# Optimization experiments

Measured on AMD Instinct MI355X. Metric: run time of the kernel, lower is better.

## Reference

```python
import jax, jax.numpy as jnp
import numpy as np

B, N = 32, 512
N_DIM, N_P, N_K = 128, 3, 2
F0_DIM = N_DIM * N_P            # 384
CAT_DIM = N_DIM * (N_K + 1) * N_P  # 1152


def setup_inputs() -> dict:
    key = jax.random.key(0)
    ks = jax.random.split(key, 12)
    s = 0.05
    return {
        "loc": jax.random.uniform(ks[0], (B, N, 2), dtype=jnp.float32),
        "deadline": jax.random.uniform(ks[1], (B, N), dtype=jnp.float32),
        "workload": jax.random.uniform(ks[2], (B, N), dtype=jnp.float32),
        "depot": jax.random.uniform(ks[3], (B, 1, 2), dtype=jnp.float32),
        "W_init": jax.random.normal(ks[4], (3, F0_DIM), dtype=jnp.float32) * s,
        "b_init": jnp.zeros((F0_DIM,), jnp.float32),
        "W_dep": jax.random.normal(ks[5], (2, N_DIM), dtype=jnp.float32) * s,
        "b_dep": jnp.zeros((N_DIM,), jnp.float32),
        "W_g1": jax.random.normal(ks[6], (CAT_DIM, N_DIM), dtype=jnp.float32) * s,
        "b_g1": jnp.zeros((N_DIM,), jnp.float32),
        "W_g2": jax.random.normal(ks[7], (CAT_DIM, N_DIM), dtype=jnp.float32) * s,
        "b_g2": jnp.zeros((N_DIM,), jnp.float32),
        "W_g3": jax.random.normal(ks[8], (CAT_DIM, N_DIM), dtype=jnp.float32) * s,
        "b_g3": jnp.zeros((N_DIM,), jnp.float32),
        "gamma": jnp.ones((F0_DIM,), jnp.float32),
        "beta": jnp.zeros((F0_DIM,), jnp.float32),
        "W_F": jax.random.normal(ks[9], (F0_DIM, N_DIM), dtype=jnp.float32) * s,
        "b_F": jnp.zeros((N_DIM,), jnp.float32),
    }


def _forward(loc, deadline, workload, depot, W_init, b_init, W_dep, b_dep,
             W_g1, b_g1, W_g2, b_g2, W_g3, b_g3, gamma, beta, W_F, b_F):
    # X = [loc, deadline/deadline.max()] -> [B,N,3] (workload is concatenated then dropped in original)
    X = jnp.concatenate([loc, (deadline / deadline.max())[..., None]], axis=-1)
    n = X.shape[1]
    # pairwise squared distances [B,N,N]
    d2 = ((X[:, :, None, :] - X[:, None, :, :]) ** 2).sum(-1)
    off = ~jnp.eye(n, dtype=bool)                      # off-diagonal mask
    d2_safe = jnp.where(off, d2, 1.0)
    A = jnp.where(off, 1.0 / jnp.sqrt(d2_safe), 0.0)   # A = 1/dist off-diag, 0 on diag
    A = jnp.where(jnp.isnan(A), 0.0, A)                # A[A!=A]=0
    A = A / A.max()                                    # global max-normalize
    deg = A.sum(-1) - 1.0                              # (A.sum(-1) - 1)
    L = jnp.eye(n, dtype=A.dtype) * deg[:, None, :] - A  # D - A (diag = deg)
    L2 = L @ L

    F0 = X @ W_init + b_init                           # [B,N,384]
    F0_sq = F0 * F0
    F0_cu = F0 * F0_sq

    def prop(F):
        return jnp.concatenate([F, L @ F, L2 @ F], axis=-1)  # [B,N,1152]

    g1 = prop(F0) @ W_g1 + b_g1
    g2 = prop(F0_sq) @ W_g2 + b_g2
    g3 = prop(F0_cu) @ W_g3 + b_g3
    F1 = jnp.concatenate([g1, g2, g3], axis=-1)        # [B,N,384]
    F1 = jax.nn.leaky_relu(F1) + F0

    # BatchNorm1d (training mode): stats over flattened (B*N) samples, biased var
    flat = F1.reshape(-1, F1.shape[-1])
    mu = flat.mean(0)
    var = ((flat - mu) ** 2).mean(0)
    F1 = (F1 - mu) / jnp.sqrt(var + 1e-5) * gamma + beta

    F_final = jax.nn.leaky_relu(F1 @ W_F + b_F)        # [B,N,128]
    dep = depot @ W_dep + b_dep                        # [B,1,128]
    h = jnp.concatenate([dep, F_final], axis=1)        # [B,N+1,128]
    return h, h.mean(axis=1)


def reference(loc, deadline, workload, depot, W_init, b_init, W_dep, b_dep,
              W_g1, b_g1, W_g2, b_g2, W_g3, b_g3, gamma, beta, W_F, b_F):
    return _forward(loc, deadline, workload, depot, W_init, b_init, W_dep, b_dep,
                    W_g1, b_g1, W_g2, b_g2, W_g3, b_g3, gamma, beta, W_F, b_F)
```

## Files before the change

### kernel.cpp

```cpp
#include <hip/hip_runtime.h>

#define LEAKY(x) ((x) > 0.0f ? (x) : 0.01f * (x))

typedef __attribute__((ext_vector_type(8))) short bf16x8;
typedef __attribute__((ext_vector_type(4))) float f32x4;
typedef __attribute__((ext_vector_type(4))) unsigned short u16x4;

__device__ __forceinline__ unsigned short f2bf(float f) {
    unsigned int u = __float_as_uint(f);
    unsigned int r = (u + 0x7fffu + ((u >> 16) & 1u)) >> 16;
    return (unsigned short)r;
}
__device__ __forceinline__ float bf2f(unsigned short u) {
    return __uint_as_float(((unsigned int)u) << 16);
}

__device__ __forceinline__ void dma16(const unsigned short* g, unsigned short* l) {
    __builtin_amdgcn_global_load_lds(
        (const __attribute__((address_space(1))) void*)g,
        (__attribute__((address_space(3))) void*)l, 16, 0, 0);
}


__global__ void k_dmax(const float* __restrict__ deadline, float* __restrict__ dmax) {
    __shared__ float red[256];
    int t = threadIdx.x;
    float m = -1e30f;
    for (int i = t; i < 16384; i += 256) m = fmaxf(m, deadline[i]);
    red[t] = m; __syncthreads();
    for (int s = 128; s > 0; s >>= 1) {
        if (t < s) red[t] = fmaxf(red[t], red[t + s]);
        __syncthreads();
    }
    if (t == 0) *dmax = red[0];
}

__global__ __launch_bounds__(256) void k_buildR(const float* __restrict__ loc,
                                                const float* __restrict__ deadline,
                                                const float* __restrict__ dmaxv,
                                                float* __restrict__ R,
                                                float* __restrict__ rowsum, float* __restrict__ pmax) {
    int blk = blockIdx.x;
    int wave = threadIdx.x >> 6, lane = threadIdx.x & 63;
    int bi = blk * 4 + wave;
    int b = bi >> 9, i = bi & 511;
    float invd = 1.0f / (*dmaxv);
    const float* lb = loc + b * 1024;
    const float* db = deadline + b * 512;
    float xi = lb[i * 2], yi = lb[i * 2 + 1], zi = db[i] * invd;
    float lsum = 0.f, lmax = 0.f;
    float* Rrow = R + (size_t)bi * 512;
    for (int j = lane; j < 512; j += 64) {
        float d0 = xi - lb[j * 2], d1 = yi - lb[j * 2 + 1], d2 = zi - db[j] * invd;
        float dd = d0 * d0 + d1 * d1 + d2 * d2;
        float r = (j == i) ? 0.f : rsqrtf(dd);
        Rrow[j] = r;
        lsum += r; lmax = fmaxf(lmax, r);
    }
    for (int off = 32; off > 0; off >>= 1) {
        lsum += __shfl_down(lsum, off);
        lmax = fmaxf(lmax, __shfl_down(lmax, off));
    }
    __shared__ float smax[4];
    if (lane == 0) { rowsum[bi] = lsum; smax[wave] = lmax; }
    __syncthreads();
    if (threadIdx.x == 0) pmax[blk] = fmaxf(fmaxf(smax[0], smax[1]), fmaxf(smax[2], smax[3]));
}

__global__ void k_amax(const float* __restrict__ pmax, float* __restrict__ amaxf) {
    __shared__ float red[256];
    int t = threadIdx.x;
    float m = 0.f;
    for (int i = t; i < 4096; i += 256) m = fmaxf(m, pmax[i]);
    red[t] = m; __syncthreads();
    for (int s = 128; s > 0; s >>= 1) {
        if (t < s) red[t] = fmaxf(red[t], red[t + s]);
        __syncthreads();
    }
    if (t == 0) *amaxf = red[0];
}

__global__ void k_buildL(const float* __restrict__ R, const float* __restrict__ rowsum,
                         const float* __restrict__ amaxf, unsigned short* __restrict__ Lb) {
    int id = blockIdx.x * 256 + threadIdx.x;
    float inv = 1.0f / (*amaxf);
    size_t e = (size_t)id * 4;
    size_t bi = e >> 9;
    int i = (int)(bi & 511);
    int j0 = (int)(e & 511);
    float4 rv = *(const float4*)(R + e);
    float diag = rowsum[bi] * inv - 1.0f;
    u16x4 o;
    o[0] = f2bf(i == j0     ? diag : -rv.x * inv);
    o[1] = f2bf(i == j0 + 1 ? diag : -rv.y * inv);
    o[2] = f2bf(i == j0 + 2 ? diag : -rv.z * inv);
    o[3] = f2bf(i == j0 + 3 ? diag : -rv.w * inv);
    *(u16x4*)(Lb + e) = o;
}

__global__ void k_F0pow(const float* __restrict__ loc, const float* __restrict__ deadline,
                        const float* __restrict__ dmaxv,
                        const float* __restrict__ Wi, const float* __restrict__ bi_,
                        unsigned short* __restrict__ P1, unsigned short* __restrict__ P2,
                        unsigned short* __restrict__ P3) {
    int id = blockIdx.x * 256 + threadIdx.x;
    int row = id / 96, c4 = (id % 96) * 4;
    float x0 = loc[row * 2], x1 = loc[row * 2 + 1], x2 = deadline[row] / (*dmaxv);
    float4 w0 = *(const float4*)(Wi + c4);
    float4 w1 = *(const float4*)(Wi + 384 + c4);
    float4 w2 = *(const float4*)(Wi + 768 + c4);
    float4 bb = *(const float4*)(bi_ + c4);
    float f[4] = {x0 * w0.x + x1 * w1.x + x2 * w2.x + bb.x,
                  x0 * w0.y + x1 * w1.y + x2 * w2.y + bb.y,
                  x0 * w0.z + x1 * w1.z + x2 * w2.z + bb.z,
                  x0 * w0.w + x1 * w1.w + x2 * w2.w + bb.w};
    u16x4 o1, o2, o3;
#pragma unroll
    for (int j = 0; j < 4; j++) {
        o1[j] = f2bf(f[j]); o2[j] = f2bf(f[j] * f[j]); o3[j] = f2bf(f[j] * f[j] * f[j]);
    }
    size_t e = (size_t)row * 384 + c4;
    *(u16x4*)(P1 + e) = o1; *(u16x4*)(P2 + e) = o2; *(u16x4*)(P3 + e) = o3;
}

__global__ void k_prepW(const float* __restrict__ Wg1, const float* __restrict__ Wg2,
                        const float* __restrict__ Wg3, unsigned short* __restrict__ WgT) {
    int id = blockIdx.x * 256 + threadIdx.x;
    int combo = id / 49152, rem = id % 49152;
    int n = rem / 384, k = rem % 384;
    int kp = combo / 3, part = combo % 3;
    const float* W = (kp == 0) ? Wg1 : (kp == 1 ? Wg2 : Wg3);
    WgT[id] = f2bf(W[(part * 384 + k) * 128 + n]);
}


__device__ __forceinline__ void phase128x64(
    const unsigned short* __restrict__ Ab, int Astr,
    const unsigned short* __restrict__ Bb, int Bstr,
    int kiters, unsigned short* AsL, unsigned short* BsL,
    f32x4 (&acc)[4][2], int t)
{
    const int wave = t >> 6, lane = t & 63;
    const int wm = wave >> 1, wn = wave & 1;
    const int quad = lane >> 4, l16 = lane & 15;
    const int lrow = lane >> 2, lkq = (lane & 3) * 8;
    for (int s = 0; s < kiters; s++) {
        __syncthreads();
        int k0 = s * 64;
#pragma unroll
        for (int h = 0; h < 2; h++) {
            const unsigned short* Ah = Ab + k0 + h * 32 + lkq;
            unsigned short* Ap = AsL + h * 4096;
            dma16(Ah + (size_t)(wave * 16 + lrow) * Astr, Ap + wave * 512);
            dma16(Ah + (size_t)((wave + 4) * 16 + lrow) * Astr, Ap + (wave + 4) * 512);
            dma16(Bb + k0 + h * 32 + lkq + (size_t)(wave * 16 + lrow) * Bstr,
                  BsL + h * 2048 + wave * 512);
        }
        __syncthreads();
#pragma unroll
        for (int h = 0; h < 2; h++) {
            bf16x8 af[4], bfr[2];
#pragma unroll
            for (int i = 0; i < 4; i++)
                af[i] = *(const bf16x8*)(AsL + h * 4096 + (wm * 64 + i * 16 + l16) * 32 + quad * 8);
#pragma unroll
            for (int n = 0; n < 2; n++)
                bfr[n] = *(const bf16x8*)(BsL + h * 2048 + (wn * 32 + n * 16 + l16) * 32 + quad * 8);
#pragma unroll
            for (int i = 0; i < 4; i++)
#pragma unroll
                for (int n = 0; n < 2; n++)
                    acc[i][n] = __builtin_amdgcn_mfma_f32_16x16x32_bf16(af[i], bfr[n], acc[i][n], 0, 0, 0);
        }
    }
}

__device__ __forceinline__ void phase64x64(
    const unsigned short* __restrict__ Ab, int Astr,
    const unsigned short* __restrict__ Bb, int Bstr,
    int kiters, unsigned short* AsL, unsigned short* BsL,
    f32x4 (&acc)[2][2], int t)
{
    const int wave = t >> 6, lane = t & 63;
    const int wm = wave >> 1, wn = wave & 1;
    const int quad = lane >> 4, l16 = lane & 15;
    const int lrow = lane >> 2, lkq = (lane & 3) * 8;
    for (int s = 0; s < kiters; s++) {
        __syncthreads();
        int k0 = s * 64;
#pragma unroll
        for (int h = 0; h < 2; h++) {
            dma16(Ab + k0 + h * 32 + lkq + (size_t)(wave * 16 + lrow) * Astr,
                  AsL + h * 2048 + wave * 512);
            dma16(Bb + k0 + h * 32 + lkq + (size_t)(wave * 16 + lrow) * Bstr,
                  BsL + h * 2048 + wave * 512);
        }
        __syncthreads();
#pragma unroll
        for (int h = 0; h < 2; h++) {
            bf16x8 af[2], bfr[2];
#pragma unroll
            for (int i = 0; i < 2; i++)
                af[i] = *(const bf16x8*)(AsL + h * 2048 + (wm * 32 + i * 16 + l16) * 32 + quad * 8);
#pragma unroll
            for (int n = 0; n < 2; n++)
                bfr[n] = *(const bf16x8*)(BsL + h * 2048 + (wn * 32 + n * 16 + l16) * 32 + quad * 8);
#pragma unroll
            for (int i = 0; i < 2; i++)
#pragma unroll
                for (int n = 0; n < 2; n++)
                    acc[i][n] = __builtin_amdgcn_mfma_f32_16x16x32_bf16(af[i], bfr[n], acc[i][n], 0, 0, 0);
        }
    }
}

__global__ __launch_bounds__(256) void k_ygemmT(
    const unsigned short* __restrict__ WgT,
    const unsigned short* __restrict__ P1, const unsigned short* __restrict__ P2,
    const unsigned short* __restrict__ P3, unsigned short* __restrict__ Y2T)
{
    __shared__ unsigned short AsL[8192], BsL[4096];
    const int t = threadIdx.x;
    const int kp = blockIdx.x;
    const int nb = blockIdx.y;
    const int b = blockIdx.z;
    const unsigned short* P = (kp == 0) ? P1 : (kp == 1 ? P2 : P3);
    f32x4 acc[4][2];
#pragma unroll
    for (int i = 0; i < 4; i++)
#pragma unroll
        for (int n = 0; n < 2; n++) acc[i][n] = (f32x4){0.f, 0.f, 0.f, 0.f};
    phase128x64(WgT + (size_t)(kp * 3 + 2) * 49152, 384,
                P + ((size_t)b * 512 + nb * 64) * 384, 384, 6, AsL, BsL, acc, t);

    const int wave = t >> 6, lane = t & 63;
    const int wm = wave >> 1, wn = wave & 1;
    const int quad = lane >> 4, l16 = lane & 15;
#pragma unroll
    for (int i = 0; i < 4; i++)
#pragma unroll
        for (int n = 0; n < 2; n++) {
            int g = kp * 128 + wm * 64 + i * 16 + quad * 4;
            int node = nb * 64 + wn * 32 + n * 16 + l16;
#pragma unroll
            for (int r = 0; r < 4; r++)
                Y2T[((size_t)b * 384 + g + r) * 512 + node] = f2bf(acc[i][n][r]);
        }
}

__global__ __launch_bounds__(256) void k_lg1T(
    const unsigned short* __restrict__ Lb, const unsigned short* __restrict__ Y2T,
    const unsigned short* __restrict__ WgT,
    const unsigned short* __restrict__ P1, const unsigned short* __restrict__ P2,
    const unsigned short* __restrict__ P3, unsigned short* __restrict__ ZT)
{
    __shared__ unsigned short AsL[8192], BsL[4096];
    const int t = threadIdx.x;
    const int kp = blockIdx.x;
    const int nb = blockIdx.y;
    const int b = blockIdx.z;
    const unsigned short* P = (kp == 0) ? P1 : (kp == 1 ? P2 : P3);
    f32x4 acc[4][2];
#pragma unroll
    for (int i = 0; i < 4; i++)
#pragma unroll
        for (int n = 0; n < 2; n++) acc[i][n] = (f32x4){0.f, 0.f, 0.f, 0.f};
    phase128x64(Y2T + (size_t)b * 196608 + (size_t)kp * 128 * 512, 512,
                Lb + (size_t)b * 262144 + (size_t)nb * 64 * 512, 512, 8, AsL, BsL, acc, t);
    phase128x64(WgT + (size_t)(kp * 3 + 1) * 49152, 384,
                P + ((size_t)b * 512 + nb * 64) * 384, 384, 6, AsL, BsL, acc, t);

    const int wave = t >> 6, lane = t & 63;
    const int wm = wave >> 1, wn = wave & 1;
    const int quad = lane >> 4, l16 = lane & 15;
#pragma unroll
    for (int i = 0; i < 4; i++)
#pragma unroll
        for (int n = 0; n < 2; n++) {
            int g = kp * 128 + wm * 64 + i * 16 + quad * 4;
            int node = nb * 64 + wn * 32 + n * 16 + l16;
#pragma unroll
            for (int r = 0; r < 4; r++)
                ZT[((size_t)b * 384 + g + r) * 512 + node] = f2bf(acc[i][n][r]);
        }
}

__global__ __launch_bounds__(256) void k_lg2(
    const unsigned short* __restrict__ Lb, const unsigned short* __restrict__ ZT,
    const unsigned short* __restrict__ WgT,
    const unsigned short* __restrict__ P1, const unsigned short* __restrict__ P2,
    const unsigned short* __restrict__ P3,
    const float* __restrict__ bg1, const float* __restrict__ bg2, const float* __restrict__ bg3,
    unsigned short* __restrict__ F1b, float* __restrict__ bn1, float* __restrict__ bn2)
{
    __shared__ unsigned short AsL[8192], BsL[4096];
    __shared__ float bnS[64], bnQ[64];
    const int t = threadIdx.x;
    const int mb = blockIdx.x;
    const int gt = blockIdx.y;
    const int b = blockIdx.z;
    const int kp = gt >> 1;
    if (t < 64) { bnS[t] = 0.f; bnQ[t] = 0.f; }
    const unsigned short* P = (kp == 0) ? P1 : (kp == 1 ? P2 : P3);
    f32x4 acc[4][2];
#pragma unroll
    for (int i = 0; i < 4; i++)
#pragma unroll
        for (int n = 0; n < 2; n++) acc[i][n] = (f32x4){0.f, 0.f, 0.f, 0.f};
    phase128x64(Lb + (size_t)b * 262144 + (size_t)mb * 128 * 512, 512,
                ZT + (size_t)b * 196608 + (size_t)gt * 64 * 512, 512, 8, AsL, BsL, acc, t);
    phase128x64(P + ((size_t)b * 512 + mb * 128) * 384, 384,
                WgT + (size_t)(kp * 3) * 49152 + (size_t)(gt & 1) * 64 * 384, 384, 6, AsL, BsL, acc, t);

    const int wave = t >> 6, lane = t & 63;
    const int wm = wave >> 1, wn = wave & 1;
    const int quad = lane >> 4, l16 = lane & 15;
    const float* bg = (kp == 0) ? bg1 : (kp == 1 ? bg2 : bg3);
    float ls1[2], ls2[2];
#pragma unroll
    for (int n = 0; n < 2; n++) { ls1[n] = 0.f; ls2[n] = 0.f; }
#pragma unroll
    for (int i = 0; i < 4; i++) {
        int rowl = mb * 128 + wm * 64 + i * 16 + quad * 4;
        size_t rowg = (size_t)b * 512 + rowl;
#pragma unroll
        for (int n = 0; n < 2; n++) {
            int nloc = wn * 32 + n * 16 + l16;
            int g = gt * 64 + nloc;
            float bias = bg[(gt & 1) * 64 + nloc];
#pragma unroll
            for (int r = 0; r < 4; r++) {
                size_t idx = (rowg + r) * 384 + g;
                float c = acc[i][n][r] + bias;
                float v = LEAKY(c) + bf2f(P1[idx]);
                F1b[idx] = f2bf(v);
                ls1[n] += v; ls2[n] += v * v;
            }
        }
    }
#pragma unroll
    for (int n = 0; n < 2; n++) {
        int nloc = wn * 32 + n * 16 + l16;
        atomicAdd(&bnS[nloc], ls1[n]);
        atomicAdd(&bnQ[nloc], ls2[n]);
    }
    __syncthreads();
    if (t < 64) {
        atomicAdd(&bn1[gt * 64 + t], bnS[t]);
        atomicAdd(&bn2[gt * 64 + t], bnQ[t]);
    }
}

__global__ __launch_bounds__(384) void k_bnfin_beff(
    const float* __restrict__ bn1, const float* __restrict__ bn2,
    const float* __restrict__ gamma, const float* __restrict__ beta,
    const float* __restrict__ WF, const float* __restrict__ bF,
    float* __restrict__ sS, float* __restrict__ beffv)
{
    __shared__ float ttL[384];
    int c = threadIdx.x;
    float mu = bn1[c] * (1.f / 16384.f);
    float var = bn2[c] * (1.f / 16384.f) - mu * mu;
    float sc = gamma[c] / sqrtf(var + 1e-5f);
    sS[c] = sc;
    ttL[c] = beta[c] - mu * sc;
    __syncthreads();
    if (c < 128) {
        float a = bF[c];
        for (int k = 0; k < 384; k++) a += ttL[k] * WF[k * 128 + c];
        beffv[c] = a;
    }
}

__global__ void k_fold(const float* __restrict__ WF, const float* __restrict__ sS,
                       unsigned short* __restrict__ WFsT) {
    int id = blockIdx.x * 256 + threadIdx.x;
    int n = id / 384, k = id % 384;
    WFsT[id] = f2bf(WF[k * 128 + n] * sS[k]);
}

__global__ __launch_bounds__(256) void k_fgemm(
    const unsigned short* __restrict__ F1b, const unsigned short* __restrict__ WFsT,
    const float* __restrict__ beffv, float* __restrict__ out, float* __restrict__ msum)
{
    __shared__ unsigned short AsL[4096], BsL[4096];
    __shared__ float msS[64];
    const int t = threadIdx.x;
    const int mb = blockIdx.x;
    const int nt = blockIdx.y;
    if (t < 64) msS[t] = 0.f;
    f32x4 acc[2][2];
#pragma unroll
    for (int i = 0; i < 2; i++)
#pragma unroll
        for (int n = 0; n < 2; n++) acc[i][n] = (f32x4){0.f, 0.f, 0.f, 0.f};
    phase64x64(F1b + (size_t)mb * 64 * 384, 384,
               WFsT + (size_t)nt * 64 * 384, 384, 6, AsL, BsL, acc, t);

    const int wave = t >> 6, lane = t & 63;
    const int wm = wave >> 1, wn = wave & 1;
    const int quad = lane >> 4, l16 = lane & 15;
    const int bloc = mb >> 3;
    float ls[2];
#pragma unroll
    for (int n = 0; n < 2; n++) ls[n] = 0.f;
#pragma unroll
    for (int i = 0; i < 2; i++) {
        int rowg = mb * 64 + wm * 32 + i * 16 + quad * 4;
        int nd = rowg & 511;
#pragma unroll
        for (int n = 0; n < 2; n++) {
            int nloc = wn * 32 + n * 16 + l16;
            int col = nt * 64 + nloc;
            float bb = beffv[col];
#pragma unroll
            for (int r = 0; r < 4; r++) {
                float x = acc[i][n][r] + bb;
                float v = LEAKY(x);
                out[(size_t)bloc * 65664 + (size_t)(nd + r + 1) * 128 + col] = v;
                ls[n] += v;
            }
        }
    }
#pragma unroll
    for (int n = 0; n < 2; n++) atomicAdd(&msS[wn * 32 + n * 16 + l16], ls[n]);
    __syncthreads();
    if (t < 64) atomicAdd(&msum[bloc * 128 + nt * 64 + t], msS[t]);
}

__global__ void k_meandep(const float* __restrict__ depot, const float* __restrict__ Wd,
                          const float* __restrict__ bd, const float* __restrict__ msum,
                          float* __restrict__ out) {
    int id = blockIdx.x * 256 + threadIdx.x;
    int b = id >> 7, o = id & 127;
    float dep = depot[b * 2] * Wd[o] + depot[b * 2 + 1] * Wd[128 + o] + bd[o];
    out[(size_t)b * 65664 + o] = dep;
    out[2101248 + id] = (msum[id] + dep) * (1.0f / 513.0f);
}


extern "C" void kernel_launch(void* const* d_in, const int* in_sizes, int n_in,
                              void* d_out, int out_size, void* d_ws, size_t ws_size,
                              hipStream_t stream) {
    const float* loc      = (const float*)d_in[0];
    const float* deadline = (const float*)d_in[1];
    const float* depot    = (const float*)d_in[3];
    const float* W_init   = (const float*)d_in[4];
    const float* b_init   = (const float*)d_in[5];
    const float* W_dep    = (const float*)d_in[6];
    const float* b_dep    = (const float*)d_in[7];
    const float* W_g1     = (const float*)d_in[8];
    const float* b_g1     = (const float*)d_in[9];
    const float* W_g2     = (const float*)d_in[10];
    const float* b_g2     = (const float*)d_in[11];
    const float* W_g3     = (const float*)d_in[12];
    const float* b_g3     = (const float*)d_in[13];
    const float* gamma    = (const float*)d_in[14];
    const float* beta     = (const float*)d_in[15];
    const float* W_F      = (const float*)d_in[16];
    const float* b_F      = (const float*)d_in[17];
    float* out = (float*)d_out;
    float* ws  = (float*)d_ws;

    float* dmaxv  = ws + 0;
    float* amaxf  = ws + 4;
    float* bn1    = ws + 8;
    float* bn2    = ws + 392;
    float* msum   = ws + 776;
    float* rowsum = ws + 4872;
    float* pmax   = ws + 21256;
    float* sS     = ws + 25352;
    float* beffv  = ws + 25736;
    float* R      = ws + 25864;
    unsigned short* Lb   = (unsigned short*)(ws + 8414472);
    unsigned short* P1   = (unsigned short*)(ws + 12608776);
    unsigned short* P2   = (unsigned short*)(ws + 15754504);
    unsigned short* P3   = (unsigned short*)(ws + 18900232);
    unsigned short* WgT  = (unsigned short*)(ws + 22045960);
    unsigned short* WFsT = (unsigned short*)(ws + 22267144);
    unsigned short* Y2T  = (unsigned short*)(ws + 22291720);
    unsigned short* ZT   = (unsigned short*)(ws + 25437448);
    unsigned short* F1b  = (unsigned short*)(ws + 28583176);

    hipMemsetAsync(bn1, 0, (384 + 384 + 4096) * sizeof(float), stream);

    k_dmax<<<1, 256, 0, stream>>>(deadline, dmaxv);
    k_buildR<<<4096, 256, 0, stream>>>(loc, deadline, dmaxv, R, rowsum, pmax);
    k_amax<<<1, 256, 0, stream>>>(pmax, amaxf);
    k_buildL<<<8192, 256, 0, stream>>>(R, rowsum, amaxf, Lb);
    k_F0pow<<<6144, 256, 0, stream>>>(loc, deadline, dmaxv, W_init, b_init, P1, P2, P3);
    k_prepW<<<1728, 256, 0, stream>>>(W_g1, W_g2, W_g3, WgT);

    k_ygemmT<<<dim3(3, 8, 32), 256, 0, stream>>>(WgT, P1, P2, P3, Y2T);
    k_lg1T<<<dim3(3, 8, 32), 256, 0, stream>>>(Lb, Y2T, WgT, P1, P2, P3, ZT);
    k_lg2<<<dim3(4, 6, 32), 256, 0, stream>>>(Lb, ZT, WgT, P1, P2, P3,
                                              b_g1, b_g2, b_g3, F1b, bn1, bn2);

    k_bnfin_beff<<<1, 384, 0, stream>>>(bn1, bn2, gamma, beta, W_F, b_F, sS, beffv);
    k_fold<<<192, 256, 0, stream>>>(W_F, sS, WFsT);
    k_fgemm<<<dim3(256, 2), 256, 0, stream>>>(F1b, WFsT, beffv, out, msum);
    k_meandep<<<16, 256, 0, stream>>>(depot, W_dep, b_dep, msum, out);
}
```

Measured before the change: 265.7 us.

## Double-buffer GEMM tiles via registers, swizzle LDS, recompute distances, remap grids

The GEMM inner loops swap direct global-to-LDS DMA for register prefetch into double-buffered, XOR-swizzled shared memory, so the next K-tile loads while MFMAs run and there is one barrier per step. The two GEMM phases in each kernel are merged into one continuous pipeline. The dense fp32 distance matrix R is no longer written; the L builder recomputes rsqrt distances from loc and deadline, which removes a large global write and read. Grids are flattened with batch as the fastest index to change block scheduling and cache locality, at the cost of doubled shared memory per block.

```diff
diff --git a/kernel.cpp b/kernel.cpp
--- a/kernel.cpp
+++ b/kernel.cpp
@@ -4,6 +4,7 @@
 
 typedef __attribute__((ext_vector_type(8))) short bf16x8;
 typedef __attribute__((ext_vector_type(4))) float f32x4;
+typedef __attribute__((ext_vector_type(8))) unsigned short u16x8;
 typedef __attribute__((ext_vector_type(4))) unsigned short u16x4;
 
 __device__ __forceinline__ unsigned short f2bf(float f) {
@@ -13,12 +14,6 @@
 }
 __device__ __forceinline__ float bf2f(unsigned short u) {
     return __uint_as_float(((unsigned int)u) << 16);
-}
-
-__device__ __forceinline__ void dma16(const unsigned short* g, unsigned short* l) {
-    __builtin_amdgcn_global_load_lds(
-        (const __attribute__((address_space(1))) void*)g,
-        (__attribute__((address_space(3))) void*)l, 16, 0, 0);
 }
 
 
@@ -35,11 +30,10 @@
     if (t == 0) *dmax = red[0];
 }
 
-__global__ __launch_bounds__(256) void k_buildR(const float* __restrict__ loc,
-                                                const float* __restrict__ deadline,
-                                                const float* __restrict__ dmaxv,
-                                                float* __restrict__ R,
-                                                float* __restrict__ rowsum, float* __restrict__ pmax) {
+__global__ __launch_bounds__(256) void k_rowstats(const float* __restrict__ loc,
+                                                  const float* __restrict__ deadline,
+                                                  const float* __restrict__ dmaxv,
+                                                  float* __restrict__ rowsum, float* __restrict__ pmax) {
     int blk = blockIdx.x;
     int wave = threadIdx.x >> 6, lane = threadIdx.x & 63;
     int bi = blk * 4 + wave;
@@ -49,12 +43,10 @@
     const float* db = deadline + b * 512;
     float xi = lb[i * 2], yi = lb[i * 2 + 1], zi = db[i] * invd;
     float lsum = 0.f, lmax = 0.f;
-    float* Rrow = R + (size_t)bi * 512;
     for (int j = lane; j < 512; j += 64) {
         float d0 = xi - lb[j * 2], d1 = yi - lb[j * 2 + 1], d2 = zi - db[j] * invd;
         float dd = d0 * d0 + d1 * d1 + d2 * d2;
         float r = (j == i) ? 0.f : rsqrtf(dd);
-        Rrow[j] = r;
         lsum += r; lmax = fmaxf(lmax, r);
     }
     for (int off = 32; off > 0; off >>= 1) {
@@ -80,21 +72,35 @@
     if (t == 0) *amaxf = red[0];
 }
 
-__global__ void k_buildL(const float* __restrict__ R, const float* __restrict__ rowsum,
+__global__ void k_buildL(const float* __restrict__ loc, const float* __restrict__ deadline,
+                         const float* __restrict__ dmaxv, const float* __restrict__ rowsum,
                          const float* __restrict__ amaxf, unsigned short* __restrict__ Lb) {
     int id = blockIdx.x * 256 + threadIdx.x;
     float inv = 1.0f / (*amaxf);
+    float invd = 1.0f / (*dmaxv);
     size_t e = (size_t)id * 4;
     size_t bi = e >> 9;
+    int b = (int)(bi >> 9);
     int i = (int)(bi & 511);
     int j0 = (int)(e & 511);
-    float4 rv = *(const float4*)(R + e);
+    const float* lb = loc + b * 1024;
+    const float* db = deadline + b * 512;
+    float xi = lb[i * 2], yi = lb[i * 2 + 1], zi = db[i] * invd;
+    float4 l01 = *(const float4*)(lb + j0 * 2);
+    float4 l23 = *(const float4*)(lb + j0 * 2 + 4);
+    float4 dj = *(const float4*)(db + j0);
     float diag = rowsum[bi] * inv - 1.0f;
+    float jx[4] = {l01.x, l01.z, l23.x, l23.z};
+    float jy[4] = {l01.y, l01.w, l23.y, l23.w};
+    float jz[4] = {dj.x * invd, dj.y * invd, dj.z * invd, dj.w * invd};
     u16x4 o;
-    o[0] = f2bf(i == j0     ? diag : -rv.x * inv);
-    o[1] = f2bf(i == j0 + 1 ? diag : -rv.y * inv);
-    o[2] = f2bf(i == j0 + 2 ? diag : -rv.z * inv);
-    o[3] = f2bf(i == j0 + 3 ? diag : -rv.w * inv);
+#pragma unroll
+    for (int j = 0; j < 4; j++) {
+        float d0 = xi - jx[j], d1 = yi - jy[j], d2 = zi - jz[j];
+        float dd = d0 * d0 + d1 * d1 + d2 * d2;
+        float v = (i == j0 + j) ? diag : -rsqrtf(dd) * inv;
+        o[j] = f2bf(v);
+    }
     *(u16x4*)(Lb + e) = o;
 }
 
@@ -134,83 +140,114 @@
 }
 
 
-__device__ __forceinline__ void phase128x64(
-    const unsigned short* __restrict__ Ab, int Astr,
-    const unsigned short* __restrict__ Bb, int Bstr,
-    int kiters, unsigned short* AsL, unsigned short* BsL,
+__device__ __forceinline__ void pipe128x64(
+    const unsigned short* __restrict__ A0, int As0, const unsigned short* __restrict__ B0, int Bs0, int it0,
+    const unsigned short* __restrict__ A1, int As1, const unsigned short* __restrict__ B1, int Bs1, int it1,
+    unsigned short* AsL, unsigned short* BsL,
     f32x4 (&acc)[4][2], int t)
 {
-    const int wave = t >> 6, lane = t & 63;
+    const int lane = t & 63, wave = t >> 6;
     const int wm = wave >> 1, wn = wave & 1;
     const int quad = lane >> 4, l16 = lane & 15;
-    const int lrow = lane >> 2, lkq = (lane & 3) * 8;
-    for (int s = 0; s < kiters; s++) {
+    const int ra = t >> 1, ca = (t & 1) * 4;
+    const int rb = t >> 2, cb = (t & 3) * 2;
+    const unsigned short* Ar0 = A0 + (size_t)ra * As0;
+    const unsigned short* Ar1 = A1 ? (A1 + (size_t)ra * As1) : Ar0;
+    const unsigned short* Br0 = B0 + (size_t)rb * Bs0;
+    const unsigned short* Br1 = B1 ? (B1 + (size_t)rb * Bs1) : Br0;
+    const int total = it0 + it1;
+    u16x8 pa[4], pb[2];
+#pragma unroll
+    for (int j = 0; j < 4; j++) pa[j] = *(const u16x8*)(Ar0 + (ca + j) * 8);
+#pragma unroll
+    for (int j = 0; j < 2; j++) pb[j] = *(const u16x8*)(Br0 + (cb + j) * 8);
+    int buf = 0;
+    for (int s = 0; s < total; s++) {
+#pragma unroll
+        for (int j = 0; j < 4; j++)
+            *(u16x8*)(AsL + buf * 8192 + ra * 64 + (((ca + j) ^ (ra & 7)) * 8)) = pa[j];
+#pragma unroll
+        for (int j = 0; j < 2; j++)
+            *(u16x8*)(BsL + buf * 4096 + rb * 64 + (((cb + j) ^ (rb & 7)) * 8)) = pb[j];
         __syncthreads();
-        int k0 = s * 64;
-#pragma unroll
-        for (int h = 0; h < 2; h++) {
-            const unsigned short* Ah = Ab + k0 + h * 32 + lkq;
-            unsigned short* Ap = AsL + h * 4096;
-            dma16(Ah + (size_t)(wave * 16 + lrow) * Astr, Ap + wave * 512);
-            dma16(Ah + (size_t)((wave + 4) * 16 + lrow) * Astr, Ap + (wave + 4) * 512);
-            dma16(Bb + k0 + h * 32 + lkq + (size_t)(wave * 16 + lrow) * Bstr,
-                  BsL + h * 2048 + wave * 512);
-        }
-        __syncthreads();
+        if (s + 1 < total) {
+            int s2 = s + 1;
+            int sg = (s2 >= it0);
+            int k0 = (sg ? (s2 - it0) : s2) * 64;
+            const unsigned short* Ar = sg ? Ar1 : Ar0;
+            const unsigned short* Br = sg ? Br1 : Br0;
+#pragma unroll
+            for (int j = 0; j < 4; j++) pa[j] = *(const u16x8*)(Ar + k0 + (ca + j) * 8);
+#pragma unroll
+            for (int j = 0; j < 2; j++) pb[j] = *(const u16x8*)(Br + k0 + (cb + j) * 8);
+        }
 #pragma unroll
         for (int h = 0; h < 2; h++) {
             bf16x8 af[4], bfr[2];
+            int phys = ((h * 4 + quad) ^ (l16 & 7)) * 8;
 #pragma unroll
             for (int i = 0; i < 4; i++)
-                af[i] = *(const bf16x8*)(AsL + h * 4096 + (wm * 64 + i * 16 + l16) * 32 + quad * 8);
+                af[i] = *(const bf16x8*)(AsL + buf * 8192 + (wm * 64 + i * 16 + l16) * 64 + phys);
 #pragma unroll
             for (int n = 0; n < 2; n++)
-                bfr[n] = *(const bf16x8*)(BsL + h * 2048 + (wn * 32 + n * 16 + l16) * 32 + quad * 8);
+                bfr[n] = *(const bf16x8*)(BsL + buf * 4096 + (wn * 32 + n * 16 + l16) * 64 + phys);
 #pragma unroll
             for (int i = 0; i < 4; i++)
 #pragma unroll
                 for (int n = 0; n < 2; n++)
                     acc[i][n] = __builtin_amdgcn_mfma_f32_16x16x32_bf16(af[i], bfr[n], acc[i][n], 0, 0, 0);
         }
-    }
-}
-
-__device__ __forceinline__ void phase64x64(
-    const unsigned short* __restrict__ Ab, int Astr,
-    const unsigned short* __restrict__ Bb, int Bstr,
-    int kiters, unsigned short* AsL, unsigned short* BsL,
+        buf ^= 1;
+    }
+}
+
+__device__ __forceinline__ void pipe64x64(
+    const unsigned short* __restrict__ A0, int As0, const unsigned short* __restrict__ B0, int Bs0, int it0,
+    unsigned short* AsL, unsigned short* BsL,
     f32x4 (&acc)[2][2], int t)
 {
-    const int wave = t >> 6, lane = t & 63;
+    const int lane = t & 63, wave = t >> 6;
     const int wm = wave >> 1, wn = wave & 1;
     const int quad = lane >> 4, l16 = lane & 15;
-    const int lrow = lane >> 2, lkq = (lane & 3) * 8;
-    for (int s = 0; s < kiters; s++) {
+    const int rb = t >> 2, cb = (t & 3) * 2;
+    const unsigned short* Ar0 = A0 + (size_t)rb * As0;
+    const unsigned short* Br0 = B0 + (size_t)rb * Bs0;
+    u16x8 pa[2], pb[2];
+#pragma unroll
+    for (int j = 0; j < 2; j++) { pa[j] = *(const u16x8*)(Ar0 + (cb + j) * 8);
+                                  pb[j] = *(const u16x8*)(Br0 + (cb + j) * 8); }
+    int buf = 0;
+    for (int s = 0; s < it0; s++) {
+#pragma unroll
+        for (int j = 0; j < 2; j++) {
+            int phys = ((cb + j) ^ (rb & 7)) * 8;
+            *(u16x8*)(AsL + buf * 4096 + rb * 64 + phys) = pa[j];
+            *(u16x8*)(BsL + buf * 4096 + rb * 64 + phys) = pb[j];
+        }
         __syncthreads();
-        int k0 = s * 64;
-#pragma unroll
-        for (int h = 0; h < 2; h++) {
-            dma16(Ab + k0 + h * 32 + lkq + (size_t)(wave * 16 + lrow) * Astr,
-                  AsL + h * 2048 + wave * 512);
-            dma16(Bb + k0 + h * 32 + lkq + (size_t)(wave * 16 + lrow) * Bstr,
-                  BsL + h * 2048 + wave * 512);
-        }
-        __syncthreads();
+        if (s + 1 < it0) {
+            int k0 = (s + 1) * 64;
+#pragma unroll
+            for (int j = 0; j < 2; j++) { pa[j] = *(const u16x8*)(Ar0 + k0 + (cb + j) * 8);
+                                          pb[j] = *(const u16x8*)(Br0 + k0 + (cb + j) * 8); }
+        }
 #pragma unroll
         for (int h = 0; h < 2; h++) {
             bf16x8 af[2], bfr[2];
+            int phys = ((h * 4 + quad) ^ (l16 & 7)) * 8;
 #pragma unroll
             for (int i = 0; i < 2; i++)
-                af[i] = *(const bf16x8*)(AsL + h * 2048 + (wm * 32 + i * 16 + l16) * 32 + quad * 8);
+                af[i] = *(const bf16x8*)(AsL + buf * 4096 + (wm * 32 + i * 16 + l16) * 64 + phys);
 #pragma unroll
             for (int n = 0; n < 2; n++)
-                bfr[n] = *(const bf16x8*)(BsL + h * 2048 + (wn * 32 + n * 16 + l16) * 32 + quad * 8);
+                bfr[n] = *(const bf16x8*)(BsL + buf * 4096 + (wn * 32 + n * 16 + l16) * 64 + phys);
 #pragma unroll
             for (int i = 0; i < 2; i++)
 #pragma unroll
                 for (int n = 0; n < 2; n++)
                     acc[i][n] = __builtin_amdgcn_mfma_f32_16x16x32_bf16(af[i], bfr[n], acc[i][n], 0, 0, 0);
         }
+        buf ^= 1;
     }
 }
 
@@ -219,19 +256,20 @@
     const unsigned short* __restrict__ P1, const unsigned short* __restrict__ P2,
     const unsigned short* __restrict__ P3, unsigned short* __restrict__ Y2T)
 {
-    __shared__ unsigned short AsL[8192], BsL[4096];
+    __shared__ unsigned short AsL[16384], BsL[8192];
     const int t = threadIdx.x;
-    const int kp = blockIdx.x;
-    const int nb = blockIdx.y;
-    const int b = blockIdx.z;
+    const int id = blockIdx.x;
+    const int b = id & 31, tt = id >> 5;
+    const int kp = tt >> 3, nb = tt & 7;
     const unsigned short* P = (kp == 0) ? P1 : (kp == 1 ? P2 : P3);
     f32x4 acc[4][2];
 #pragma unroll
     for (int i = 0; i < 4; i++)
 #pragma unroll
         for (int n = 0; n < 2; n++) acc[i][n] = (f32x4){0.f, 0.f, 0.f, 0.f};
-    phase128x64(WgT + (size_t)(kp * 3 + 2) * 49152, 384,
-                P + ((size_t)b * 512 + nb * 64) * 384, 384, 6, AsL, BsL, acc, t);
+    pipe128x64(WgT + (size_t)(kp * 3 + 2) * 49152, 384,
+               P + ((size_t)b * 512 + nb * 64) * 384, 384, 6,
+               nullptr, 0, nullptr, 0, 0, AsL, BsL, acc, t);
 
     const int wave = t >> 6, lane = t & 63;
     const int wm = wave >> 1, wn = wave & 1;
@@ -254,21 +292,21 @@
     const unsigned short* __restrict__ P1, const unsigned short* __restrict__ P2,
     const unsigned short* __restrict__ P3, unsigned short* __restrict__ ZT)
 {
-    __shared__ unsigned short AsL[8192], BsL[4096];
+    __shared__ unsigned short AsL[16384], BsL[8192];
     const int t = threadIdx.x;
-    const int kp = blockIdx.x;
-    const int nb = blockIdx.y;
-    const int b = blockIdx.z;
+    const int id = blockIdx.x;
+    const int b = id & 31, tt = id >> 5;
+    const int kp = tt >> 3, nb = tt & 7;
     const unsigned short* P = (kp == 0) ? P1 : (kp == 1 ? P2 : P3);
     f32x4 acc[4][2];
 #pragma unroll
     for (int i = 0; i < 4; i++)
 #pragma unroll
         for (int n = 0; n < 2; n++) acc[i][n] = (f32x4){0.f, 0.f, 0.f, 0.f};
-    phase128x64(Y2T + (size_t)b * 196608 + (size_t)kp * 128 * 512, 512,
-                Lb + (size_t)b * 262144 + (size_t)nb * 64 * 512, 512, 8, AsL, BsL, acc, t);
-    phase128x64(WgT + (size_t)(kp * 3 + 1) * 49152, 384,
-                P + ((size_t)b * 512 + nb * 64) * 384, 384, 6, AsL, BsL, acc, t);
+    pipe128x64(Y2T + (size_t)b * 196608 + (size_t)kp * 128 * 512, 512,
+               Lb + (size_t)b * 262144 + (size_t)nb * 64 * 512, 512, 8,
+               WgT + (size_t)(kp * 3 + 1) * 49152, 384,
+               P + ((size_t)b * 512 + nb * 64) * 384, 384, 6, AsL, BsL, acc, t);
 
     const int wave = t >> 6, lane = t & 63;
     const int wm = wave >> 1, wn = wave & 1;
@@ -293,12 +331,12 @@
     const float* __restrict__ bg1, const float* __restrict__ bg2, const float* __restrict__ bg3,
     unsigned short* __restrict__ F1b, float* __restrict__ bn1, float* __restrict__ bn2)
 {
-    __shared__ unsigned short AsL[8192], BsL[4096];
+    __shared__ unsigned short AsL[16384], BsL[8192];
     __shared__ float bnS[64], bnQ[64];
     const int t = threadIdx.x;
-    const int mb = blockIdx.x;
-    const int gt = blockIdx.y;
-    const int b = blockIdx.z;
+    const int id = blockIdx.x;
+    const int b = id & 31, tt = id >> 5;
+    const int mb = tt & 3, gt = tt >> 2;
     const int kp = gt >> 1;
     if (t < 64) { bnS[t] = 0.f; bnQ[t] = 0.f; }
     const unsigned short* P = (kp == 0) ? P1 : (kp == 1 ? P2 : P3);
@@ -307,10 +345,11 @@
     for (int i = 0; i < 4; i++)
 #pragma unroll
         for (int n = 0; n < 2; n++) acc[i][n] = (f32x4){0.f, 0.f, 0.f, 0.f};
-    phase128x64(Lb + (size_t)b * 262144 + (size_t)mb * 128 * 512, 512,
-                ZT + (size_t)b * 196608 + (size_t)gt * 64 * 512, 512, 8, AsL, BsL, acc, t);
-    phase128x64(P + ((size_t)b * 512 + mb * 128) * 384, 384,
-                WgT + (size_t)(kp * 3) * 49152 + (size_t)(gt & 1) * 64 * 384, 384, 6, AsL, BsL, acc, t);
+    pipe128x64(Lb + (size_t)b * 262144 + (size_t)mb * 128 * 512, 512,
+               ZT + (size_t)b * 196608 + (size_t)gt * 64 * 512, 512, 8,
+               P + ((size_t)b * 512 + mb * 128) * 384, 384,
+               WgT + (size_t)(kp * 3) * 49152 + (size_t)(gt & 1) * 64 * 384, 384, 6,
+               AsL, BsL, acc, t);
 
     const int wave = t >> 6, lane = t & 63;
     const int wm = wave >> 1, wn = wave & 1;
@@ -383,41 +422,39 @@
     const unsigned short* __restrict__ F1b, const unsigned short* __restrict__ WFsT,
     const float* __restrict__ beffv, float* __restrict__ out, float* __restrict__ msum)
 {
-    __shared__ unsigned short AsL[4096], BsL[4096];
+    __shared__ unsigned short AsL[8192], BsL[8192];
     __shared__ float msS[64];
     const int t = threadIdx.x;
-    const int mb = blockIdx.x;
-    const int nt = blockIdx.y;
+    const int id = blockIdx.x;
+    const int b = id & 31, tt = id >> 5;
+    const int seg = tt >> 1, nt = tt & 1;
     if (t < 64) msS[t] = 0.f;
     f32x4 acc[2][2];
 #pragma unroll
     for (int i = 0; i < 2; i++)
 #pragma unroll
         for (int n = 0; n < 2; n++) acc[i][n] = (f32x4){0.f, 0.f, 0.f, 0.f};
-    phase64x64(F1b + (size_t)mb * 64 * 384, 384,
-               WFsT + (size_t)nt * 64 * 384, 384, 6, AsL, BsL, acc, t);
+    pipe64x64(F1b + ((size_t)b * 512 + seg * 64) * 384, 384,
+              WFsT + (size_t)nt * 64 * 384, 384, 6, AsL, BsL, acc, t);
 
     const int wave = t >> 6, lane = t & 63;
     const int wm = wave >> 1, wn = wave & 1;
     const int quad = lane >> 4, l16 = lane & 15;
-    const int bloc = mb >> 3;
     float ls[2];
 #pragma unroll
     for (int n = 0; n < 2; n++) ls[n] = 0.f;
 #pragma unroll
     for (int i = 0; i < 2; i++) {
-        int rowg = mb * 64 + wm * 32 + i * 16 + quad * 4;
-        int nd = rowg & 511;
+        int nd = seg * 64 + wm * 32 + i * 16 + quad * 4;
 #pragma unroll
         for (int n = 0; n < 2; n++) {
-            int nloc = wn * 32 + n * 16 + l16;
-            int col = nt * 64 + nloc;
+            int col = nt * 64 + wn * 32 + n * 16 + l16;
             float bb = beffv[col];
 #pragma unroll
             for (int r = 0; r < 4; r++) {
                 float x = acc[i][n][r] + bb;
                 float v = LEAKY(x);
-                out[(size_t)bloc * 65664 + (size_t)(nd + r + 1) * 128 + col] = v;
+                out[(size_t)b * 65664 + (size_t)(nd + r + 1) * 128 + col] = v;
                 ls[n] += v;
             }
         }
@@ -425,7 +462,7 @@
 #pragma unroll
     for (int n = 0; n < 2; n++) atomicAdd(&msS[wn * 32 + n * 16 + l16], ls[n]);
     __syncthreads();
-    if (t < 64) atomicAdd(&msum[bloc * 128 + nt * 64 + t], msS[t]);
+    if (t < 64) atomicAdd(&msum[b * 128 + nt * 64 + t], msS[t]);
 }
 
 __global__ void k_meandep(const float* __restrict__ depot, const float* __restrict__ Wd,
@@ -471,33 +508,32 @@
     float* pmax   = ws + 21256;
     float* sS     = ws + 25352;
     float* beffv  = ws + 25736;
-    float* R      = ws + 25864;
-    unsigned short* Lb   = (unsigned short*)(ws + 8414472);
-    unsigned short* P1   = (unsigned short*)(ws + 12608776);
-    unsigned short* P2   = (unsigned short*)(ws + 15754504);
-    unsigned short* P3   = (unsigned short*)(ws + 18900232);
-    unsigned short* WgT  = (unsigned short*)(ws + 22045960);
-    unsigned short* WFsT = (unsigned short*)(ws + 22267144);
-    unsigned short* Y2T  = (unsigned short*)(ws + 22291720);
-    unsigned short* ZT   = (unsigned short*)(ws + 25437448);
-    unsigned short* F1b  = (unsigned short*)(ws + 28583176);
+    unsigned short* Lb   = (unsigned short*)(ws + 25864);
+    unsigned short* P1   = (unsigned short*)(ws + 4220168);
+    unsigned short* P2   = (unsigned short*)(ws + 7365896);
+    unsigned short* P3   = (unsigned short*)(ws + 10511624);
+    unsigned short* WgT  = (unsigned short*)(ws + 13657352);
+    unsigned short* WFsT = (unsigned short*)(ws + 13878536);
+    unsigned short* Y2T  = (unsigned short*)(ws + 13903112);
+    unsigned short* ZT   = (unsigned short*)(ws + 17048840);
+    unsigned short* F1b  = (unsigned short*)(ws + 20194568);
 
     hipMemsetAsync(bn1, 0, (384 + 384 + 4096) * sizeof(float), stream);
 
     k_dmax<<<1, 256, 0, stream>>>(deadline, dmaxv);
-    k_buildR<<<4096, 256, 0, stream>>>(loc, deadline, dmaxv, R, rowsum, pmax);
+    k_rowstats<<<4096, 256, 0, stream>>>(loc, deadline, dmaxv, rowsum, pmax);
     k_amax<<<1, 256, 0, stream>>>(pmax, amaxf);
-    k_buildL<<<8192, 256, 0, stream>>>(R, rowsum, amaxf, Lb);
+    k_buildL<<<8192, 256, 0, stream>>>(loc, deadline, dmaxv, rowsum, amaxf, Lb);
     k_F0pow<<<6144, 256, 0, stream>>>(loc, deadline, dmaxv, W_init, b_init, P1, P2, P3);
     k_prepW<<<1728, 256, 0, stream>>>(W_g1, W_g2, W_g3, WgT);
 
-    k_ygemmT<<<dim3(3, 8, 32), 256, 0, stream>>>(WgT, P1, P2, P3, Y2T);
-    k_lg1T<<<dim3(3, 8, 32), 256, 0, stream>>>(Lb, Y2T, WgT, P1, P2, P3, ZT);
-    k_lg2<<<dim3(4, 6, 32), 256, 0, stream>>>(Lb, ZT, WgT, P1, P2, P3,
-                                              b_g1, b_g2, b_g3, F1b, bn1, bn2);
+    k_ygemmT<<<768, 256, 0, stream>>>(WgT, P1, P2, P3, Y2T);
+    k_lg1T<<<768, 256, 0, stream>>>(Lb, Y2T, WgT, P1, P2, P3, ZT);
+    k_lg2<<<768, 256, 0, stream>>>(Lb, ZT, WgT, P1, P2, P3,
+                                   b_g1, b_g2, b_g3, F1b, bn1, bn2);
 
     k_bnfin_beff<<<1, 384, 0, stream>>>(bn1, bn2, gamma, beta, W_F, b_F, sS, beffv);
     k_fold<<<192, 256, 0, stream>>>(W_F, sS, WFsT);
-    k_fgemm<<<dim3(256, 2), 256, 0, stream>>>(F1b, WFsT, beffv, out, msum);
+    k_fgemm<<<512, 256, 0, stream>>>(F1b, WFsT, beffv, out, msum);
     k_meandep<<<16, 256, 0, stream>>>(depot, W_dep, b_dep, msum, out);
 }
```

After: 236.9 us. -10.8%, faster.
